# Kernel optimization log

Measured on AMD Instinct MI355X. Metric: run time of the kernel, lower is better.

The kernel has to match this reference:

```python
import jax, jax.numpy as jnp
import numpy as np

N = 10000
E = 160000
H = 4
NEG_SLOPE = 0.2


def _edge_softmax(e, dst):
    # e: [E, H] logits; softmax over edges sharing the same dst node
    m = jax.ops.segment_max(e, dst, num_segments=N)          # [N, H]
    m = jnp.where(jnp.isfinite(m), m, 0.0)
    ex = jnp.exp(e - m[dst])                                  # [E, H]
    den = jax.ops.segment_sum(ex, dst, num_segments=N)       # [N, H]
    return ex / (den[dst] + 1e-9)


def _gat_layer(x, src, dst, W, al, ar, resW, edge=None, We=None, ae=None):
    # x: [N, Fin]; W: [Fin, H, D]; al/ar/ae: [H, D]; resW: [Fin, D]
    feat = jnp.einsum('ni,ihd->nhd', x, W)                    # [N, H, D]
    el = jnp.einsum('nhd,hd->nh', feat, al)                   # [N, H]
    er = jnp.einsum('nhd,hd->nh', feat, ar)                   # [N, H]
    e = el[src] + er[dst]                                     # [E, H]
    if edge is not None:
        ef = jnp.einsum('ei,ihd->ehd', edge, We)              # [E, H, D]
        e = e + jnp.einsum('ehd,hd->eh', ef, ae)
    e = jax.nn.leaky_relu(e, NEG_SLOPE)
    alpha = _edge_softmax(e, dst)                             # [E, H]
    msg = feat[src] * alpha[:, :, None]                       # [E, H, D]
    out = jax.ops.segment_sum(msg, dst, num_segments=N)      # [N, H, D]
    return out.mean(axis=1) + x @ resW                        # [N, D]


def setup_inputs() -> dict:
    key = jax.random.key(0)
    ks = jax.random.split(key, 24)
    node_in, edge_in, hid, out = 128, 64, 128, 256
    s = 0.1
    d = {
        'node_feats': jax.random.normal(ks[0], (N, node_in), jnp.float32),
        'edge_feats': jax.random.normal(ks[1], (E, edge_in), jnp.float32),
        'src': jax.random.randint(ks[2], (E,), 0, N, jnp.int32),
        'dst': jax.random.randint(ks[3], (E,), 0, N, jnp.int32),
        # conv1 (with edge feats): node_in -> hid
        'W1':  s * jax.random.normal(ks[4],  (node_in, H, hid), jnp.float32),
        'We1': s * jax.random.normal(ks[5],  (edge_in, H, hid), jnp.float32),
        'al1': s * jax.random.normal(ks[6],  (H, hid), jnp.float32),
        'ar1': s * jax.random.normal(ks[7],  (H, hid), jnp.float32),
        'ae1': s * jax.random.normal(ks[8],  (H, hid), jnp.float32),
        'res1': s * jax.random.normal(ks[9], (node_in, hid), jnp.float32),
        # conv2: hid -> hid
        'W2':  s * jax.random.normal(ks[10], (hid, H, hid), jnp.float32),
        'al2': s * jax.random.normal(ks[11], (H, hid), jnp.float32),
        'ar2': s * jax.random.normal(ks[12], (H, hid), jnp.float32),
        'res2': s * jax.random.normal(ks[13], (hid, hid), jnp.float32),
        # conv3: hid -> hid
        'W3':  s * jax.random.normal(ks[14], (hid, H, hid), jnp.float32),
        'al3': s * jax.random.normal(ks[15], (H, hid), jnp.float32),
        'ar3': s * jax.random.normal(ks[16], (H, hid), jnp.float32),
        'res3': s * jax.random.normal(ks[17], (hid, hid), jnp.float32),
        # conv4: hid -> out
        'W4':  s * jax.random.normal(ks[18], (hid, H, out), jnp.float32),
        'al4': s * jax.random.normal(ks[19], (H, out), jnp.float32),
        'ar4': s * jax.random.normal(ks[20], (H, out), jnp.float32),
        'res4': s * jax.random.normal(ks[21], (hid, out), jnp.float32),
    }
    return d


def reference(node_feats, edge_feats, src, dst,
              W1, We1, al1, ar1, ae1, res1,
              W2, al2, ar2, res2,
              W3, al3, ar3, res3,
              W4, al4, ar4, res4):
    h = jax.nn.relu(_gat_layer(node_feats, src, dst, W1, al1, ar1, res1,
                               edge=edge_feats, We=We1, ae=ae1))
    h = jax.nn.relu(_gat_layer(h, src, dst, W2, al2, ar2, res2))
    h = jax.nn.relu(_gat_layer(h, src, dst, W3, al3, ar3, res3))
    h = jax.nn.relu(_gat_layer(h, src, dst, W4, al4, ar4, res4))
    return h
```

## Files before the change

kernel.cpp:

```cpp
#include <hip/hip_runtime.h>

#define NN 10000
#define EE 160000

#define HB 625
#define GYR 157
#define GB128 (11 * GYR)
#define GB256 (21 * GYR)

typedef __attribute__((ext_vector_type(8))) short bf16x8;
typedef __attribute__((ext_vector_type(4))) float f32x4;
typedef __attribute__((ext_vector_type(2))) float f32x2;
typedef __attribute__((ext_vector_type(8))) float f32x8;
typedef __attribute__((ext_vector_type(16))) float f32x16;

__device__ __forceinline__ short f2b(float f) {
    union { float f; unsigned u; } v; v.f = f;
    unsigned r = v.u + 0x7FFF + ((v.u >> 16) & 1);
    return (short)(r >> 16);
}
__device__ __forceinline__ unsigned char f2q(float f) {
    return (unsigned char)(__builtin_amdgcn_cvt_pk_fp8_f32(f, f, 0, false) & 0xFF);
}

struct PrepParams {
    const float* tsrc[8];
    short* tdst[8];
    int tN[8];
    int tshift[8];
    int tcum4[9];
    const float* W[4]; const float* al[4]; const float* ar[4];
    short* Wc[4]; int Dl[4]; int base[4];
    const float* We1; const float* ae1; float* vbuf;
    const float* node_feats; short* xb;
    const int* dst; int* counts;
    int bWA, bV, bC, bZ, nblk;
};
__global__ __launch_bounds__(256) void prep_kernel(PrepParams P) {
    int blk = blockIdx.x, tid = threadIdx.x;
    if (blk < P.bWA) {
        int t = blk * 256 + tid;
        if (t >= P.tcum4[8]) return;
        int i = 0;
        #pragma unroll
        for (int j = 1; j < 8; ++j) i += (t >= P.tcum4[j]);
        int local = t - P.tcum4[i];
        int N = P.tN[i], sh = P.tshift[i];
        int k = local >> (sh - 2);
        int nq = local & ((N >> 2) - 1);
        float4 v = *(const float4*)(P.tsrc[i] + (size_t)k * N + nq * 4);
        short* d = P.tdst[i] + (size_t)nq * 4 * 128 + k;
        d[0] = f2b(v.x); d[128] = f2b(v.y); d[256] = f2b(v.z); d[384] = f2b(v.w);
    } else if (blk < P.bV) {
        int bl = blk - P.bWA;
        int l = bl >> 7, within = bl & 127;
        int wv = tid >> 6, ln = tid & 63;
        int wid = within * 4 + wv;
        int k = wid >> 2, h = wid & 3;
        int D = P.Dl[l];
        const float* w = P.W[l] + ((size_t)k * 4 + h) * D;
        const float* a = P.al[l] + (size_t)h * D;
        const float* r = P.ar[l] + (size_t)h * D;
        float sa, sr;
        if (D == 128) {
            float2 w2 = ((const float2*)w)[ln];
            float2 a2 = ((const float2*)a)[ln];
            float2 r2 = ((const float2*)r)[ln];
            sa = w2.x * a2.x + w2.y * a2.y;
            sr = w2.x * r2.x + w2.y * r2.y;
        } else {
            float4 w4 = ((const float4*)w)[ln];
            float4 a4 = ((const float4*)a)[ln];
            float4 r4 = ((const float4*)r)[ln];
            sa = w4.x * a4.x + w4.y * a4.y + w4.z * a4.z + w4.w * a4.w;
            sr = w4.x * r4.x + w4.y * r4.y + w4.z * r4.z + w4.w * r4.w;
        }
        #pragma unroll
        for (int o = 32; o; o >>= 1) { sa += __shfl_xor(sa, o); sr += __shfl_xor(sr, o); }
        if (ln == 0) {
            P.Wc[l][(size_t)(P.base[l] + h) * 128 + k]     = f2b(sa);
            P.Wc[l][(size_t)(P.base[l] + 4 + h) * 128 + k] = f2b(sr);
        }
    } else if (blk < P.bC) {
        int bl = blk - P.bV;
        int wv = tid >> 6, ln = tid & 63;
        int i = bl * 4 + wv;
        #pragma unroll
        for (int h = 0; h < 4; ++h) {
            const float* w = P.We1 + ((size_t)i * 4 + h) * 128;
            const float* a = P.ae1 + (size_t)h * 128;
            float2 w2 = ((const float2*)w)[ln];
            float2 a2 = ((const float2*)a)[ln];
            float s = w2.x * a2.x + w2.y * a2.y;
            #pragma unroll
            for (int o = 32; o; o >>= 1) s += __shfl_xor(s, o);
            if (ln == 0) P.vbuf[i * 4 + h] = s;
        }
    } else if (blk < P.bZ) {
        int t = (blk - P.bC) * 256 + tid;
        if (t < NN * 32) {
            float4 v = ((const float4*)P.node_feats)[t];
            uint2 pk;
            pk.x = (unsigned short)f2b(v.x) | ((unsigned)(unsigned short)f2b(v.y) << 16);
            pk.y = (unsigned short)f2b(v.z) | ((unsigned)(unsigned short)f2b(v.w) << 16);
            ((uint2*)P.xb)[t] = pk;
        }
    } else {
        int e = (blk - P.bZ) * 256 + tid;
        if (e < EE) atomicAdd(&P.counts[P.dst[e]], 1);
    }
}

template <int D>
__device__ __forceinline__ void gemm_body(const short* __restrict__ A,
                                          const short* __restrict__ Bt,
                                          unsigned char* __restrict__ featq,
                                          float* __restrict__ y,
                                          float* __restrict__ elr,
                                          int M, int bx, int by) {
    constexpr int HD = 4 * D;
    int wave = threadIdx.x >> 6, lane = threadIdx.x & 63;
    int m0 = by * 64;
    int n0 = bx * 64 + wave * 16;
    int r = lane & 15, quad = lane >> 4;
    f32x4 acc[4] = {};
    const short* bp = Bt + (size_t)(n0 + r) * 128 + quad * 8;
    #pragma unroll
    for (int k0 = 0; k0 < 128; k0 += 32) {
        bf16x8 bfrag = *(const bf16x8*)(bp + k0);
        #pragma unroll
        for (int mt = 0; mt < 4; ++mt) {
            int gm = m0 + mt * 16 + r;
            bf16x8 afrag = {};
            if (gm < M) afrag = *(const bf16x8*)(A + (size_t)gm * 128 + k0 + quad * 8);
            acc[mt] = __builtin_amdgcn_mfma_f32_16x16x32_bf16(afrag, bfrag, acc[mt], 0, 0, 0);
        }
    }
    int col = n0 + r;
    #pragma unroll
    for (int mt = 0; mt < 4; ++mt) {
        #pragma unroll
        for (int rr = 0; rr < 4; ++rr) {
            int gm = m0 + mt * 16 + quad * 4 + rr;
            if (gm >= M) continue;
            float v = acc[mt][rr];
            if (col < HD)              featq[(size_t)gm * HD + col] = f2q(v);
            else if (col < HD + D)     y[(size_t)gm * D + (col - HD)] = v;
            else if (col < HD + D + 8) elr[(size_t)gm * 8 + (col - HD - D)] = v;
        }
    }
}

template <int D>
__global__ __launch_bounds__(256) void gemm_fused(const short* __restrict__ A,
                                                  const short* __restrict__ Bt,
                                                  unsigned char* __restrict__ featq,
                                                  float* __restrict__ y,
                                                  float* __restrict__ elr,
                                                  int M) {
    gemm_body<D>(A, Bt, featq, y, elr, M, blockIdx.x, blockIdx.y);
}

__device__ __forceinline__ void scan_body(const int* __restrict__ counts,
                                          int* __restrict__ off,
                                          int* __restrict__ cur,
                                          int* __restrict__ nodeperm) {
    __shared__ int part[256];
    __shared__ int hist[64], hbase[64], hcnt[64];
    const int n = NN;
    int tid = threadIdx.x;
    if (tid < 64) { hist[tid] = 0; hcnt[tid] = 0; }
    __syncthreads();
    int lo = tid * 40;
    int4 r[10];
    int s = 0;
    #pragma unroll
    for (int q = 0; q < 10; ++q) {
        int idx = lo + q * 4;
        int4 v = make_int4(0, 0, 0, 0);
        if (idx + 3 < n) v = *(const int4*)(counts + idx);
        r[q] = v;
        s += v.x + v.y + v.z + v.w;
        atomicAdd(&hist[v.x < 63 ? v.x : 63], 1);
        atomicAdd(&hist[v.y < 63 ? v.y : 63], 1);
        atomicAdd(&hist[v.z < 63 ? v.z : 63], 1);
        atomicAdd(&hist[v.w < 63 ? v.w : 63], 1);
    }
    part[tid] = s;
    __syncthreads();
    for (int o = 1; o < 256; o <<= 1) {
        int v = (tid >= o) ? part[tid - o] : 0;
        __syncthreads();
        part[tid] += v;
        __syncthreads();
    }
    int run = tid ? part[tid - 1] : 0;
    #pragma unroll
    for (int q = 0; q < 10; ++q) {
        int4 v = r[q], o4;
        o4.x = run; run += v.x;
        o4.y = run; run += v.y;
        o4.z = run; run += v.z;
        o4.w = run; run += v.w;
        int idx = lo + q * 4;
        if (idx + 3 < n) { *(int4*)(off + idx) = o4; *(int4*)(cur + idx) = o4; }
    }
    if (tid == 255) off[n] = part[255];
    if (tid < 64) {
        int acc = 0;
        for (int b2 = tid + 1; b2 < 64; ++b2) acc += hist[b2];
        hbase[tid] = acc;
    }
    __syncthreads();
    #pragma unroll
    for (int q = 0; q < 10; ++q) {
        int4 v = r[q];
        int idx = lo + q * 4;
        int b0 = v.x < 63 ? v.x : 63;
        int b1 = v.y < 63 ? v.y : 63;
        int b2 = v.z < 63 ? v.z : 63;
        int b3 = v.w < 63 ? v.w : 63;
        nodeperm[hbase[b0] + atomicAdd(&hcnt[b0], 1)] = idx;
        nodeperm[hbase[b1] + atomicAdd(&hcnt[b1], 1)] = idx + 1;
        nodeperm[hbase[b2] + atomicAdd(&hcnt[b2], 1)] = idx + 2;
        nodeperm[hbase[b3] + atomicAdd(&hcnt[b3], 1)] = idx + 3;
    }
}

__global__ __launch_bounds__(256) void gemm1_extra_scan(const float* __restrict__ ef,
                                                        const float* __restrict__ vbuf,
                                                        float* __restrict__ extraU,
                                                        const short* __restrict__ A,
                                                        const short* __restrict__ Bt,
                                                        unsigned char* __restrict__ featq,
                                                        float* __restrict__ y,
                                                        float* __restrict__ elr,
                                                        const int* __restrict__ counts,
                                                        int* __restrict__ off,
                                                        int* __restrict__ cur,
                                                        int* __restrict__ nodeperm) {
    int vb = blockIdx.x;
    if (vb < HB) {
        __shared__ float vs[256];
        vs[threadIdx.x] = vbuf[threadIdx.x];
        __syncthreads();
        int e = vb * 256 + threadIdx.x;
        if (e < EE) {
            float a0 = 0.f, a1 = 0.f, a2 = 0.f, a3 = 0.f;
            const float4* e4 = (const float4*)(ef + (size_t)e * 64);
            #pragma unroll
            for (int c = 0; c < 16; ++c) {
                float4 x = e4[c];
                int b = c * 16;
                a0 += x.x * vs[b + 0] + x.y * vs[b + 4] + x.z * vs[b + 8] + x.w * vs[b + 12];
                a1 += x.x * vs[b + 1] + x.y * vs[b + 5] + x.z * vs[b + 9] + x.w * vs[b + 13];
                a2 += x.x * vs[b + 2] + x.y * vs[b + 6] + x.z * vs[b + 10] + x.w * vs[b + 14];
                a3 += x.x * vs[b + 3] + x.y * vs[b + 7] + x.z * vs[b + 11] + x.w * vs[b + 15];
            }
            float4 o; o.x = a0; o.y = a1; o.z = a2; o.w = a3;
            *(float4*)(extraU + (size_t)e * 4) = o;
        }
    } else if (vb < HB + GB128) {
        int b = vb - HB;
        gemm_body<128>(A, Bt, featq, y, elr, NN, b % 11, b / 11);
    } else {
        scan_body(counts, off, cur, nodeperm);
    }
}

__global__ __launch_bounds__(256) void fill_extra(const int* __restrict__ src,
                                                  const int* __restrict__ dst,
                                                  int* __restrict__ cur,
                                                  const float* __restrict__ extraU,
                                                  int* __restrict__ ssrc,
                                                  float* __restrict__ extra, int E) {
    int e = blockIdx.x * 256 + threadIdx.x;
    if (e >= E) return;
    int p = atomicAdd(&cur[dst[e]], 1);
    ssrc[p] = src[e];
    *(float4*)(extra + (size_t)p * 4) = *(const float4*)(extraU + (size_t)e * 4);
}

__device__ __forceinline__ f32x8 accum8q(f32x8 a, uint2 v, float w) {
    f32x2 p;
    p = __builtin_amdgcn_cvt_pk_f32_fp8(v.x, false); a[0] += w * p.x; a[1] += w * p.y;
    p = __builtin_amdgcn_cvt_pk_f32_fp8(v.x, true);  a[2] += w * p.x; a[3] += w * p.y;
    p = __builtin_amdgcn_cvt_pk_f32_fp8(v.y, false); a[4] += w * p.x; a[5] += w * p.y;
    p = __builtin_amdgcn_cvt_pk_f32_fp8(v.y, true);  a[6] += w * p.x; a[7] += w * p.y;
    return a;
}
__device__ __forceinline__ f32x16 accum16q(f32x16 a, uint4 v, float w) {
    f32x2 p;
    p = __builtin_amdgcn_cvt_pk_f32_fp8(v.x, false); a[0] += w * p.x; a[1] += w * p.y;
    p = __builtin_amdgcn_cvt_pk_f32_fp8(v.x, true);  a[2] += w * p.x; a[3] += w * p.y;
    p = __builtin_amdgcn_cvt_pk_f32_fp8(v.y, false); a[4] += w * p.x; a[5] += w * p.y;
    p = __builtin_amdgcn_cvt_pk_f32_fp8(v.y, true);  a[6] += w * p.x; a[7] += w * p.y;
    p = __builtin_amdgcn_cvt_pk_f32_fp8(v.z, false); a[8] += w * p.x; a[9] += w * p.y;
    p = __builtin_amdgcn_cvt_pk_f32_fp8(v.z, true);  a[10] += w * p.x; a[11] += w * p.y;
    p = __builtin_amdgcn_cvt_pk_f32_fp8(v.w, false); a[12] += w * p.x; a[13] += w * p.y;
    p = __builtin_amdgcn_cvt_pk_f32_fp8(v.w, true);  a[14] += w * p.x; a[15] += w * p.y;
    return a;
}

struct SM64 { float ev0, ev1, ev2, ev3; int sx0, sx1, sx2, sx3; float sc; };

template <bool HAS_EXTRA>
__device__ __forceinline__ SM64 softmax64(int r0, int deg, int h, int jh, float erh,
                                          const float* __restrict__ elr,
                                          const float* __restrict__ extra,
                                          const int* __restrict__ ssrc) {
    SM64 R;
    float a0 = -1e30f, a1 = -1e30f, a2 = -1e30f, a3 = -1e30f;
    int sx0 = 0, sx1 = 0, sx2 = 0, sx3 = 0;
    auto lg = [&](int j, int& sx, float& a) {
        if (j < deg) {
            int idx = r0 + j;
            sx = ssrc[idx];
            float v = elr[(size_t)sx * 8 + h] + erh;
            if (HAS_EXTRA) v += extra[(size_t)idx * 4 + h];
            a = v > 0.f ? v : 0.2f * v;
        }
    };
    lg(jh, sx0, a0);
    if (deg > 16) lg(jh + 16, sx1, a1);
    if (deg > 32) lg(jh + 32, sx2, a2);
    if (deg > 48) lg(jh + 48, sx3, a3);
    float m = fmaxf(fmaxf(a0, a1), fmaxf(a2, a3));
    #pragma unroll
    for (int o = 1; o < 16; o <<= 1) m = fmaxf(m, __shfl_xor(m, o));
    R.ev0 = __expf(a0 - m); R.ev1 = __expf(a1 - m);
    R.ev2 = __expf(a2 - m); R.ev3 = __expf(a3 - m);
    float ss = R.ev0 + R.ev1 + R.ev2 + R.ev3;
    #pragma unroll
    for (int o = 1; o < 16; o <<= 1) ss += __shfl_xor(ss, o);
    R.sc = 0.25f / (ss + 1e-9f);
    R.sx0 = sx0; R.sx1 = sx1; R.sx2 = sx2; R.sx3 = sx3;
    return R;
}

template <bool HAS_EXTRA>
__global__ __launch_bounds__(256) void gat128(const unsigned char* __restrict__ featq,
                                              const float* __restrict__ elr,
                                              const float* __restrict__ extra,
                                              const int* __restrict__ ssrc,
                                              const int* __restrict__ off,
                                              const int* __restrict__ nodeperm,
                                              const float* __restrict__ yres,
                                              short* __restrict__ ybf) {
    int wv = threadIdx.x >> 6, ln = threadIdx.x & 63;
    int n = nodeperm[blockIdx.x * 4 + wv];
    int r0 = off[n], deg = off[n + 1] - r0;
    int h = ln >> 4, jh = ln & 15;
    float erh = elr[(size_t)n * 8 + 4 + h];
    f32x8 acc = {};
    const unsigned char* basep = featq + ln * 8;
    float sc;

    if (deg <= 64) {
        SM64 R = softmax64<HAS_EXTRA>(r0, deg, h, jh, erh, elr, extra, ssrc);
        sc = R.sc;
        int hh = h << 4;
        auto blk16 = [&](float ee, int si, int cnt) {
            int c = 0;
            for (; c + 4 <= cnt; c += 4) {
                float w0 = __shfl(ee, hh | c),       w1 = __shfl(ee, hh | (c + 1));
                float w2 = __shfl(ee, hh | (c + 2)), w3 = __shfl(ee, hh | (c + 3));
                int s0 = __shfl(si, c),     s1 = __shfl(si, c + 1);
                int s2 = __shfl(si, c + 2), s3 = __shfl(si, c + 3);
                uint2 v0 = *(const uint2*)(basep + (size_t)s0 * 512);
                uint2 v1 = *(const uint2*)(basep + (size_t)s1 * 512);
                uint2 v2 = *(const uint2*)(basep + (size_t)s2 * 512);
                uint2 v3 = *(const uint2*)(basep + (size_t)s3 * 512);
                acc = accum8q(acc, v0, w0); acc = accum8q(acc, v1, w1);
                acc = accum8q(acc, v2, w2); acc = accum8q(acc, v3, w3);
            }
            for (; c < cnt; ++c) {
                float w = __shfl(ee, hh | c);
                int s = __shfl(si, c);
                uint2 v = *(const uint2*)(basep + (size_t)s * 512);
                acc = accum8q(acc, v, w);
            }
        };
        blk16(R.ev0, R.sx0, deg < 16 ? deg : 16);
        if (deg > 16) blk16(R.ev1, R.sx1, deg < 32 ? deg - 16 : 16);
        if (deg > 32) blk16(R.ev2, R.sx2, deg < 48 ? deg - 32 : 16);
        if (deg > 48) blk16(R.ev3, R.sx3, deg - 48);
    } else {
        auto lgt = [&](int c) {
            int s = ssrc[r0 + c];
            float v = elr[(size_t)s * 8 + h] + erh;
            if (HAS_EXTRA) v += extra[(size_t)(r0 + c) * 4 + h];
            return v > 0.f ? v : 0.2f * v;
        };
        float m = -1e30f;
        for (int c = 0; c < deg; ++c) m = fmaxf(m, lgt(c));
        float ss = 0.f;
        for (int c = 0; c < deg; ++c) ss += __expf(lgt(c) - m);
        sc = 0.25f / (ss + 1e-9f);
        for (int c = 0; c < deg; ++c) {
            float w = __expf(lgt(c) - m);
            int s = ssrc[r0 + c];
            uint2 v = *(const uint2*)(basep + (size_t)s * 512);
            acc = accum8q(acc, v, w);
        }
    }

    f32x8 t;
    #pragma unroll
    for (int i = 0; i < 8; ++i) {
        float v = acc[i] * sc;
        v += __shfl_xor(v, 16);
        v += __shfl_xor(v, 32);
        t[i] = v;
    }
    if (ln < 16) {
        const float* yr = yres + (size_t)n * 128 + ln * 8;
        float4 y0 = *(const float4*)yr;
        float4 y1 = *(const float4*)(yr + 4);
        float o0 = fmaxf(y0.x + t[0], 0.f), o1 = fmaxf(y0.y + t[1], 0.f);
        float o2 = fmaxf(y0.z + t[2], 0.f), o3 = fmaxf(y0.w + t[3], 0.f);
        float o4 = fmaxf(y1.x + t[4], 0.f), o5 = fmaxf(y1.y + t[5], 0.f);
        float o6 = fmaxf(y1.z + t[6], 0.f), o7 = fmaxf(y1.w + t[7], 0.f);
        uint4 pa;
        pa.x = (unsigned short)f2b(o0) | ((unsigned)(unsigned short)f2b(o1) << 16);
        pa.y = (unsigned short)f2b(o2) | ((unsigned)(unsigned short)f2b(o3) << 16);
        pa.z = (unsigned short)f2b(o4) | ((unsigned)(unsigned short)f2b(o5) << 16);
        pa.w = (unsigned short)f2b(o6) | ((unsigned)(unsigned short)f2b(o7) << 16);
        *(uint4*)(ybf + (size_t)n * 128 + ln * 8) = pa;
    }
}

__global__ __launch_bounds__(256) void gat256(const unsigned char* __restrict__ featq,
                                              const float* __restrict__ elr,
                                              const int* __restrict__ ssrc,
                                              const int* __restrict__ off,
                                              const int* __restrict__ nodeperm,
                                              const float* __restrict__ yres,
                                              float* __restrict__ yout) {
    __shared__ float red[2][16 * 17];
    int wv = threadIdx.x >> 6, ln = threadIdx.x & 63;
    int slot = wv >> 1, half = wv & 1;
    int n = nodeperm[blockIdx.x * 2 + slot];
    int r0 = off[n], deg = off[n + 1] - r0;
    int h = ln >> 4, jh = ln & 15;
    float erh = elr[(size_t)n * 8 + 4 + h];
    f32x16 acc = {};
    const unsigned char* basep = featq + ln * 16;
    float sc;

    if (deg <= 64) {
        SM64 R = softmax64<false>(r0, deg, h, jh, erh, elr, nullptr, ssrc);
        sc = R.sc;
        int hh = h << 4;
        auto blk16 = [&](float ee, int si, int cnt) {
            int c = half;
            for (; c + 6 < cnt; c += 8) {
                float w0 = __shfl(ee, hh | c),       w1 = __shfl(ee, hh | (c + 2));
                float w2 = __shfl(ee, hh | (c + 4)), w3 = __shfl(ee, hh | (c + 6));
                int s0 = __shfl(si, c),     s1 = __shfl(si, c + 2);
                int s2 = __shfl(si, c + 4), s3 = __shfl(si, c + 6);
                uint4 v0 = *(const uint4*)(basep + (size_t)s0 * 1024);
                uint4 v1 = *(const uint4*)(basep + (size_t)s1 * 1024);
                uint4 v2 = *(const uint4*)(basep + (size_t)s2 * 1024);
                uint4 v3 = *(const uint4*)(basep + (size_t)s3 * 1024);
                acc = accum16q(acc, v0, w0); acc = accum16q(acc, v1, w1);
                acc = accum16q(acc, v2, w2); acc = accum16q(acc, v3, w3);
            }
            for (; c < cnt; c += 2) {
                float w = __shfl(ee, hh | c);
                int s = __shfl(si, c);
                uint4 v = *(const uint4*)(basep + (size_t)s * 1024);
                acc = accum16q(acc, v, w);
            }
        };
        blk16(R.ev0, R.sx0, deg < 16 ? deg : 16);
        if (deg > 16) blk16(R.ev1, R.sx1, (deg < 32 ? deg : 32) - 16);
        if (deg > 32) blk16(R.ev2, R.sx2, (deg < 48 ? deg : 48) - 32);
        if (deg > 48) blk16(R.ev3, R.sx3, deg - 48);
    } else {
        auto lgt = [&](int c) {
            int s = ssrc[r0 + c];
            float v = elr[(size_t)s * 8 + h] + erh;
            return v > 0.f ? v : 0.2f * v;
        };
        float m = -1e30f;
        for (int c = 0; c < deg; ++c) m = fmaxf(m, lgt(c));
        float ss = 0.f;
        for (int c = 0; c < deg; ++c) ss += __expf(lgt(c) - m);
        sc = 0.25f / (ss + 1e-9f);
        for (int c = half; c < deg; c += 2) {
            float w = __expf(lgt(c) - m);
            int s = ssrc[r0 + c];
            uint4 v = *(const uint4*)(basep + (size_t)s * 1024);
            acc = accum16q(acc, v, w);
        }
    }

    f32x16 t;
    #pragma unroll
    for (int i = 0; i < 16; ++i) {
        float v = acc[i] * sc;
        v += __shfl_xor(v, 16);
        v += __shfl_xor(v, 32);
        t[i] = v;
    }
    if (half == 1 && ln < 16) {
        #pragma unroll
        for (int i = 0; i < 16; ++i) red[slot][ln * 17 + i] = t[i];
    }
    __syncthreads();
    if (half == 0 && ln < 16) {
        const float* yr = yres + (size_t)n * 256 + ln * 16;
        float* yo = yout + (size_t)n * 256 + ln * 16;
        #pragma unroll
        for (int q = 0; q < 4; ++q) {
            float4 ya = *(const float4*)(yr + 4 * q);
            float4 ov;
            ov.x = fmaxf(ya.x + t[4 * q + 0] + red[slot][ln * 17 + 4 * q + 0], 0.f);
            ov.y = fmaxf(ya.y + t[4 * q + 1] + red[slot][ln * 17 + 4 * q + 1], 0.f);
            ov.z = fmaxf(ya.z + t[4 * q + 2] + red[slot][ln * 17 + 4 * q + 2], 0.f);
            ov.w = fmaxf(ya.w + t[4 * q + 3] + red[slot][ln * 17 + 4 * q + 3], 0.f);
            *(float4*)(yo + 4 * q) = ov;
        }
    }
}

extern "C" void kernel_launch(void* const* d_in, const int* in_sizes, int n_in,
                              void* d_out, int out_size, void* d_ws, size_t ws_size,
                              hipStream_t stream) {
    const float* node_feats = (const float*)d_in[0];
    const float* edge_feats = (const float*)d_in[1];
    const int*   src        = (const int*)d_in[2];
    const int*   dst        = (const int*)d_in[3];
    const float* W1   = (const float*)d_in[4];
    const float* We1  = (const float*)d_in[5];
    const float* al1  = (const float*)d_in[6];
    const float* ar1  = (const float*)d_in[7];
    const float* ae1  = (const float*)d_in[8];
    const float* res1 = (const float*)d_in[9];
    const float* W2   = (const float*)d_in[10];
    const float* al2  = (const float*)d_in[11];
    const float* ar2  = (const float*)d_in[12];
    const float* res2 = (const float*)d_in[13];
    const float* W3   = (const float*)d_in[14];
    const float* al3  = (const float*)d_in[15];
    const float* ar3  = (const float*)d_in[16];
    const float* res3 = (const float*)d_in[17];
    const float* W4   = (const float*)d_in[18];
    const float* al4  = (const float*)d_in[19];
    const float* ar4  = (const float*)d_in[20];
    const float* res4 = (const float*)d_in[21];

    char* ws = (char*)d_ws;
    auto alloc = [&](size_t bytes) -> char* {
        char* p = ws;
        ws += (bytes + 255) & ~(size_t)255;
        return p;
    };
    int*   counts  = (int*)alloc((size_t)NN * 4);
    int*   offsets = (int*)alloc((size_t)(NN + 1) * 4);
    int*   cursor  = (int*)alloc((size_t)(NN + 1) * 4);
    int*   nodeperm = (int*)alloc((size_t)NN * 4);
    int*   ssrc    = (int*)alloc((size_t)EE * 4);
    unsigned char* featq = (unsigned char*)alloc((size_t)NN * 1024);
    float* xA      = (float*)alloc((size_t)NN * 128 * 4);
    short* xb      = (short*)alloc((size_t)NN * 128 * 2);
    float* elr     = (float*)alloc((size_t)NN * 8 * 4);
    float* extra   = (float*)alloc((size_t)EE * 4 * 4);
    float* extraU  = (float*)alloc((size_t)EE * 4 * 4);
    float* vbuf    = (float*)alloc(1024);
    short* Wc1     = (short*)alloc((size_t)704 * 128 * 2);
    short* Wc2     = (short*)alloc((size_t)704 * 128 * 2);
    short* Wc3     = (short*)alloc((size_t)704 * 128 * 2);
    short* Wc4     = (short*)alloc((size_t)1344 * 128 * 2);

    PrepParams P;
    P.tsrc[0] = W1;   P.tdst[0] = Wc1;              P.tN[0] = 512;  P.tshift[0] = 9;
    P.tsrc[1] = W2;   P.tdst[1] = Wc2;              P.tN[1] = 512;  P.tshift[1] = 9;
    P.tsrc[2] = W3;   P.tdst[2] = Wc3;              P.tN[2] = 512;  P.tshift[2] = 9;
    P.tsrc[3] = W4;   P.tdst[3] = Wc4;              P.tN[3] = 1024; P.tshift[3] = 10;
    P.tsrc[4] = res1; P.tdst[4] = Wc1 + 512 * 128;  P.tN[4] = 128;  P.tshift[4] = 7;
    P.tsrc[5] = res2; P.tdst[5] = Wc2 + 512 * 128;  P.tN[5] = 128;  P.tshift[5] = 7;
    P.tsrc[6] = res3; P.tdst[6] = Wc3 + 512 * 128;  P.tN[6] = 128;  P.tshift[6] = 7;
    P.tsrc[7] = res4; P.tdst[7] = Wc4 + 1024 * 128; P.tN[7] = 256;  P.tshift[7] = 8;
    P.tcum4[0] = 0;
    for (int i = 0; i < 8; ++i) P.tcum4[i + 1] = P.tcum4[i] + P.tN[i] * 128 / 4;
    P.W[0] = W1; P.W[1] = W2; P.W[2] = W3; P.W[3] = W4;
    P.al[0] = al1; P.al[1] = al2; P.al[2] = al3; P.al[3] = al4;
    P.ar[0] = ar1; P.ar[1] = ar2; P.ar[2] = ar3; P.ar[3] = ar4;
    P.Wc[0] = Wc1; P.Wc[1] = Wc2; P.Wc[2] = Wc3; P.Wc[3] = Wc4;
    P.Dl[0] = 128; P.Dl[1] = 128; P.Dl[2] = 128; P.Dl[3] = 256;
    P.base[0] = 640; P.base[1] = 640; P.base[2] = 640; P.base[3] = 1280;
    P.We1 = We1; P.ae1 = ae1; P.vbuf = vbuf;
    P.node_feats = node_feats; P.xb = xb;
    P.dst = dst; P.counts = counts;
    P.bWA = (P.tcum4[8] + 255) / 256;
    P.bV  = P.bWA + 512;
    P.bC  = P.bV + 16;
    P.bZ  = P.bC + (NN * 32 + 255) / 256;
    P.nblk = P.bZ + HB;

    float* out = (float*)d_out;

    hipMemsetAsync(counts, 0, (size_t)NN * 4, stream);
    prep_kernel<<<P.nblk, 256, 0, stream>>>(P);
    gemm1_extra_scan<<<HB + GB128 + 1, 256, 0, stream>>>(
        edge_feats, vbuf, extraU, xb, Wc1, featq, xA, elr, counts, offsets, cursor,
        nodeperm);
    fill_extra<<<HB, 256, 0, stream>>>(src, dst, cursor, extraU, ssrc, extra, EE);

    dim3 g128(11, GYR);
    dim3 g256(21, GYR);
    gat128<true><<<NN / 4, 256, 0, stream>>>(featq, elr, extra, ssrc, offsets,
                                             nodeperm, xA, xb);
    gemm_fused<128><<<g128, 256, 0, stream>>>(xb, Wc2, featq, xA, elr, NN);
    gat128<false><<<NN / 4, 256, 0, stream>>>(featq, elr, nullptr, ssrc, offsets,
                                              nodeperm, xA, xb);
    gemm_fused<128><<<g128, 256, 0, stream>>>(xb, Wc3, featq, xA, elr, NN);
    gat128<false><<<NN / 4, 256, 0, stream>>>(featq, elr, nullptr, ssrc, offsets,
                                              nodeperm, xA, xb);
    gemm_fused<256><<<g256, 256, 0, stream>>>(xb, Wc4, featq, out, elr, NN);
    gat256<<<NN / 2, 256, 0, stream>>>(featq, elr, ssrc, offsets, nodeperm, out, out);
}
```

Baseline: 335.1 us.

## Compute edge softmax once per node and split aggregation across two waves

In gat128, each node is now handled by two wavefronts instead of one. The first wave computes the edge softmax and publishes the weights, source indices and scale through shared memory. Both waves then gather alternating edges, and their partial sums are combined through LDS before the residual add. gat256 drops its duplicated per-wave softmax and reads the shared results the same way. This trades a block-level barrier and an idle wave during the softmax phase for less redundant softmax work in gat256 and more gather parallelism in gat128.

```diff
diff --git a/kernel.cpp b/kernel.cpp
--- a/kernel.cpp
+++ b/kernel.cpp
@@ -347,26 +347,40 @@
                                               const int* __restrict__ nodeperm,
                                               const float* __restrict__ yres,
                                               short* __restrict__ ybf) {
+    __shared__ float evs[2][4][64];
+    __shared__ int   sxs[2][4][16];
+    __shared__ float scs[2][4];
+    __shared__ float tred[2][16][9];
     int wv = threadIdx.x >> 6, ln = threadIdx.x & 63;
-    int n = nodeperm[blockIdx.x * 4 + wv];
+    int slot = wv >> 1, half = wv & 1;
+    int n = nodeperm[blockIdx.x * 2 + slot];
     int r0 = off[n], deg = off[n + 1] - r0;
     int h = ln >> 4, jh = ln & 15;
-    float erh = elr[(size_t)n * 8 + 4 + h];
     f32x8 acc = {};
     const unsigned char* basep = featq + ln * 8;
-    float sc;
+    float scl = 0.f;
+
+    if (deg <= 64 && half == 0) {
+        float erh = elr[(size_t)n * 8 + 4 + h];
+        SM64 R = softmax64<HAS_EXTRA>(r0, deg, h, jh, erh, elr, extra, ssrc);
+        evs[slot][0][ln] = R.ev0; evs[slot][1][ln] = R.ev1;
+        evs[slot][2][ln] = R.ev2; evs[slot][3][ln] = R.ev3;
+        if (jh == 0) scs[slot][h] = R.sc;
+        if (ln < 16) {
+            sxs[slot][0][ln] = R.sx0; sxs[slot][1][ln] = R.sx1;
+            sxs[slot][2][ln] = R.sx2; sxs[slot][3][ln] = R.sx3;
+        }
+    }
+    __syncthreads();
 
     if (deg <= 64) {
-        SM64 R = softmax64<HAS_EXTRA>(r0, deg, h, jh, erh, elr, extra, ssrc);
-        sc = R.sc;
         int hh = h << 4;
-        auto blk16 = [&](float ee, int si, int cnt) {
-            int c = 0;
-            for (; c + 4 <= cnt; c += 4) {
-                float w0 = __shfl(ee, hh | c),       w1 = __shfl(ee, hh | (c + 1));
-                float w2 = __shfl(ee, hh | (c + 2)), w3 = __shfl(ee, hh | (c + 3));
-                int s0 = __shfl(si, c),     s1 = __shfl(si, c + 1);
-                int s2 = __shfl(si, c + 2), s3 = __shfl(si, c + 3);
+        auto blk16 = [&](const float* ev, const int* sx, int cnt) {
+            int c = half;
+            for (; c + 6 < cnt; c += 8) {
+                float w0 = ev[hh | c],       w1 = ev[hh | (c + 2)];
+                float w2 = ev[hh | (c + 4)], w3 = ev[hh | (c + 6)];
+                int s0 = sx[c], s1 = sx[c + 2], s2 = sx[c + 4], s3 = sx[c + 6];
                 uint2 v0 = *(const uint2*)(basep + (size_t)s0 * 512);
                 uint2 v1 = *(const uint2*)(basep + (size_t)s1 * 512);
                 uint2 v2 = *(const uint2*)(basep + (size_t)s2 * 512);
@@ -374,21 +388,22 @@
                 acc = accum8q(acc, v0, w0); acc = accum8q(acc, v1, w1);
                 acc = accum8q(acc, v2, w2); acc = accum8q(acc, v3, w3);
             }
-            for (; c < cnt; ++c) {
-                float w = __shfl(ee, hh | c);
-                int s = __shfl(si, c);
+            for (; c < cnt; c += 2) {
+                float w = ev[hh | c];
+                int s = sx[c];
                 uint2 v = *(const uint2*)(basep + (size_t)s * 512);
                 acc = accum8q(acc, v, w);
             }
         };
-        blk16(R.ev0, R.sx0, deg < 16 ? deg : 16);
-        if (deg > 16) blk16(R.ev1, R.sx1, deg < 32 ? deg - 16 : 16);
-        if (deg > 32) blk16(R.ev2, R.sx2, deg < 48 ? deg - 32 : 16);
-        if (deg > 48) blk16(R.ev3, R.sx3, deg - 48);
+        blk16(evs[slot][0], sxs[slot][0], deg < 16 ? deg : 16);
+        if (deg > 16) blk16(evs[slot][1], sxs[slot][1], (deg < 32 ? deg : 32) - 16);
+        if (deg > 32) blk16(evs[slot][2], sxs[slot][2], (deg < 48 ? deg : 48) - 32);
+        if (deg > 48) blk16(evs[slot][3], sxs[slot][3], deg - 48);
+        scl = scs[slot][h];
     } else {
         auto lgt = [&](int c) {
             int s = ssrc[r0 + c];
-            float v = elr[(size_t)s * 8 + h] + erh;
+            float v = elr[(size_t)s * 8 + h] + elr[(size_t)n * 8 + 4 + h];
             if (HAS_EXTRA) v += extra[(size_t)(r0 + c) * 4 + h];
             return v > 0.f ? v : 0.2f * v;
         };
@@ -396,8 +411,8 @@
         for (int c = 0; c < deg; ++c) m = fmaxf(m, lgt(c));
         float ss = 0.f;
         for (int c = 0; c < deg; ++c) ss += __expf(lgt(c) - m);
-        sc = 0.25f / (ss + 1e-9f);
-        for (int c = 0; c < deg; ++c) {
+        scl = 0.25f / (ss + 1e-9f);
+        for (int c = half; c < deg; c += 2) {
             float w = __expf(lgt(c) - m);
             int s = ssrc[r0 + c];
             uint2 v = *(const uint2*)(basep + (size_t)s * 512);
@@ -408,19 +423,28 @@
     f32x8 t;
     #pragma unroll
     for (int i = 0; i < 8; ++i) {
-        float v = acc[i] * sc;
+        float v = acc[i] * scl;
         v += __shfl_xor(v, 16);
         v += __shfl_xor(v, 32);
         t[i] = v;
     }
-    if (ln < 16) {
+    if (half == 1 && ln < 16) {
+        #pragma unroll
+        for (int i = 0; i < 8; ++i) tred[slot][ln][i] = t[i];
+    }
+    __syncthreads();
+    if (half == 0 && ln < 16) {
         const float* yr = yres + (size_t)n * 128 + ln * 8;
         float4 y0 = *(const float4*)yr;
         float4 y1 = *(const float4*)(yr + 4);
-        float o0 = fmaxf(y0.x + t[0], 0.f), o1 = fmaxf(y0.y + t[1], 0.f);
-        float o2 = fmaxf(y0.z + t[2], 0.f), o3 = fmaxf(y0.w + t[3], 0.f);
-        float o4 = fmaxf(y1.x + t[4], 0.f), o5 = fmaxf(y1.y + t[5], 0.f);
-        float o6 = fmaxf(y1.z + t[6], 0.f), o7 = fmaxf(y1.w + t[7], 0.f);
+        float o0 = fmaxf(y0.x + t[0] + tred[slot][ln][0], 0.f);
+        float o1 = fmaxf(y0.y + t[1] + tred[slot][ln][1], 0.f);
+        float o2 = fmaxf(y0.z + t[2] + tred[slot][ln][2], 0.f);
+        float o3 = fmaxf(y0.w + t[3] + tred[slot][ln][3], 0.f);
+        float o4 = fmaxf(y1.x + t[4] + tred[slot][ln][4], 0.f);
+        float o5 = fmaxf(y1.y + t[5] + tred[slot][ln][5], 0.f);
+        float o6 = fmaxf(y1.z + t[6] + tred[slot][ln][6], 0.f);
+        float o7 = fmaxf(y1.w + t[7] + tred[slot][ln][7], 0.f);
         uint4 pa;
         pa.x = (unsigned short)f2b(o0) | ((unsigned)(unsigned short)f2b(o1) << 16);
         pa.y = (unsigned short)f2b(o2) | ((unsigned)(unsigned short)f2b(o3) << 16);
@@ -438,27 +462,39 @@
                                               const float* __restrict__ yres,
                                               float* __restrict__ yout) {
     __shared__ float red[2][16 * 17];
+    __shared__ float evs[2][4][64];
+    __shared__ int   sxs[2][4][16];
+    __shared__ float scs[2][4];
     int wv = threadIdx.x >> 6, ln = threadIdx.x & 63;
     int slot = wv >> 1, half = wv & 1;
     int n = nodeperm[blockIdx.x * 2 + slot];
     int r0 = off[n], deg = off[n + 1] - r0;
     int h = ln >> 4, jh = ln & 15;
-    float erh = elr[(size_t)n * 8 + 4 + h];
     f32x16 acc = {};
     const unsigned char* basep = featq + ln * 16;
-    float sc;
+    float scl = 0.f;
+
+    if (deg <= 64 && half == 0) {
+        float erh = elr[(size_t)n * 8 + 4 + h];
+        SM64 R = softmax64<false>(r0, deg, h, jh, erh, elr, nullptr, ssrc);
+        evs[slot][0][ln] = R.ev0; evs[slot][1][ln] = R.ev1;
+        evs[slot][2][ln] = R.ev2; evs[slot][3][ln] = R.ev3;
+        if (jh == 0) scs[slot][h] = R.sc;
+        if (ln < 16) {
+            sxs[slot][0][ln] = R.sx0; sxs[slot][1][ln] = R.sx1;
+            sxs[slot][2][ln] = R.sx2; sxs[slot][3][ln] = R.sx3;
+        }
+    }
+    __syncthreads();
 
     if (deg <= 64) {
-        SM64 R = softmax64<false>(r0, deg, h, jh, erh, elr, nullptr, ssrc);
-        sc = R.sc;
         int hh = h << 4;
-        auto blk16 = [&](float ee, int si, int cnt) {
+        auto blk16 = [&](const float* ev, const int* sx, int cnt) {
             int c = half;
             for (; c + 6 < cnt; c += 8) {
-                float w0 = __shfl(ee, hh | c),       w1 = __shfl(ee, hh | (c + 2));
-                float w2 = __shfl(ee, hh | (c + 4)), w3 = __shfl(ee, hh | (c + 6));
-                int s0 = __shfl(si, c),     s1 = __shfl(si, c + 2);
-                int s2 = __shfl(si, c + 4), s3 = __shfl(si, c + 6);
+                float w0 = ev[hh | c],       w1 = ev[hh | (c + 2)];
+                float w2 = ev[hh | (c + 4)], w3 = ev[hh | (c + 6)];
+                int s0 = sx[c], s1 = sx[c + 2], s2 = sx[c + 4], s3 = sx[c + 6];
                 uint4 v0 = *(const uint4*)(basep + (size_t)s0 * 1024);
                 uint4 v1 = *(const uint4*)(basep + (size_t)s1 * 1024);
                 uint4 v2 = *(const uint4*)(basep + (size_t)s2 * 1024);
@@ -467,17 +503,19 @@
                 acc = accum16q(acc, v2, w2); acc = accum16q(acc, v3, w3);
             }
             for (; c < cnt; c += 2) {
-                float w = __shfl(ee, hh | c);
-                int s = __shfl(si, c);
+                float w = ev[hh | c];
+                int s = sx[c];
                 uint4 v = *(const uint4*)(basep + (size_t)s * 1024);
                 acc = accum16q(acc, v, w);
             }
         };
-        blk16(R.ev0, R.sx0, deg < 16 ? deg : 16);
-        if (deg > 16) blk16(R.ev1, R.sx1, (deg < 32 ? deg : 32) - 16);
-        if (deg > 32) blk16(R.ev2, R.sx2, (deg < 48 ? deg : 48) - 32);
-        if (deg > 48) blk16(R.ev3, R.sx3, deg - 48);
+        blk16(evs[slot][0], sxs[slot][0], deg < 16 ? deg : 16);
+        if (deg > 16) blk16(evs[slot][1], sxs[slot][1], (deg < 32 ? deg : 32) - 16);
+        if (deg > 32) blk16(evs[slot][2], sxs[slot][2], (deg < 48 ? deg : 48) - 32);
+        if (deg > 48) blk16(evs[slot][3], sxs[slot][3], deg - 48);
+        scl = scs[slot][h];
     } else {
+        float erh = elr[(size_t)n * 8 + 4 + h];
         auto lgt = [&](int c) {
             int s = ssrc[r0 + c];
             float v = elr[(size_t)s * 8 + h] + erh;
@@ -487,7 +525,7 @@
         for (int c = 0; c < deg; ++c) m = fmaxf(m, lgt(c));
         float ss = 0.f;
         for (int c = 0; c < deg; ++c) ss += __expf(lgt(c) - m);
-        sc = 0.25f / (ss + 1e-9f);
+        scl = 0.25f / (ss + 1e-9f);
         for (int c = half; c < deg; c += 2) {
             float w = __expf(lgt(c) - m);
             int s = ssrc[r0 + c];
@@ -499,7 +537,7 @@
     f32x16 t;
     #pragma unroll
     for (int i = 0; i < 16; ++i) {
-        float v = acc[i] * sc;
+        float v = acc[i] * scl;
         v += __shfl_xor(v, 16);
         v += __shfl_xor(v, 32);
         t[i] = v;
@@ -611,13 +649,13 @@
 
     dim3 g128(11, GYR);
     dim3 g256(21, GYR);
-    gat128<true><<<NN / 4, 256, 0, stream>>>(featq, elr, extra, ssrc, offsets,
+    gat128<true><<<NN / 2, 256, 0, stream>>>(featq, elr, extra, ssrc, offsets,
                                              nodeperm, xA, xb);
     gemm_fused<128><<<g128, 256, 0, stream>>>(xb, Wc2, featq, xA, elr, NN);
-    gat128<false><<<NN / 4, 256, 0, stream>>>(featq, elr, nullptr, ssrc, offsets,
+    gat128<false><<<NN / 2, 256, 0, stream>>>(featq, elr, nullptr, ssrc, offsets,
                                               nodeperm, xA, xb);
     gemm_fused<128><<<g128, 256, 0, stream>>>(xb, Wc3, featq, xA, elr, NN);
-    gat128<false><<<NN / 4, 256, 0, stream>>>(featq, elr, nullptr, ssrc, offsets,
+    gat128<false><<<NN / 2, 256, 0, stream>>>(featq, elr, nullptr, ssrc, offsets,
                                               nodeperm, xA, xb);
     gemm_fused<256><<<g256, 256, 0, stream>>>(xb, Wc4, featq, out, elr, NN);
     gat256<<<NN / 2, 256, 0, stream>>>(featq, elr, ssrc, offsets, nodeperm, out, out);
```

Measured after the change: 348.1 us. 3.9% more time.
